# Performance work log

Hardware: AMD Instinct MI355X
Metric: run time of the kernel (lower is better)

Reference implementation:

```python
import jax, jax.numpy as jnp
import numpy as np

WIN = 20        # max-pooling window (win_size)
OFFSET = 40     # offset_d
TRUNC = 9       # trunc_window_size
SIGMA = 4.0     # gaussian sigma
SIL = 0         # sil_idx


def _smoothing_filter():
    h = TRUNC // 2
    x = jnp.arange(-h, h + 1, dtype=jnp.float32)
    g = jnp.exp(-0.5 * (x / SIGMA) ** 2)
    g = g / g.sum()
    f = jnp.zeros(WIN, jnp.float32)
    c = WIN // 2
    return f.at[c - h:c + h + 1].set(g)


def setup_inputs() -> dict:
    key = jax.random.key(0)
    k1, k2, k3, k4 = jax.random.split(key, 4)
    B, F, C, P = 32, 8192, 256, 256
    X = jax.nn.log_softmax(jax.random.normal(k1, (B, F, C), jnp.float32), axis=-1)
    lengths = jax.random.randint(k2, (B,), 4096, F + 1)
    p_end = lengths - 100                      # phoneme end well inside the utterance
    phoneme_nums = jax.random.randint(k3, (B,), 128, P + 1)
    tgt = jax.random.randint(k4, (B, P), 1, C)  # padded phoneme labels (avoid sil=0)
    return {"X": X, "lengths": lengths, "tgt": tgt, "p_end": p_end,
            "phoneme_nums": phoneme_nums}


def reference(X, lengths, tgt, p_end, phoneme_nums):
    B, F, C = X.shape
    P = tgt.shape[1]
    filt = _smoothing_filter()

    ends_ph = jnp.minimum(p_end + OFFSET, lengths)                      # [B]
    idxs = jnp.arange(P)[None, :]                                       # [1,P]
    starts = jnp.maximum(ends_ph[:, None] - WIN * (phoneme_nums[:, None] - idxs), 0)  # [B,P]
    ends = jnp.minimum(starts + WIN, lengths[:, None])                  # [B,P]

    t = jnp.arange(WIN)
    fidx = jnp.clip(starts[:, :, None] + t, 0, F - 1)
    b_idx = jnp.arange(B)[:, None, None]
    vals = X[b_idx, fidx, tgt[:, :, None]]

    wlen = ends - starts                                                # [B,P]
    valid_t = t[None, None, :] < wlen[:, :, None]
    vals = jnp.where(valid_t, vals, 0.0)  # zeros beyond window == torch zero-pad

    # torch F.conv1d(padding='same') with even kernel: pad left 9, right 10 (cross-corr)
    lpad = (WIN - 1) // 2
    padded = jnp.pad(vals, ((0, 0), (0, 0), (lpad, WIN - 1 - lpad)))
    smoothed = jax.lax.conv_general_dilated(
        padded.reshape(B * P, 1, -1), filt.reshape(1, 1, WIN),
        window_strides=(1,), padding='VALID').reshape(B, P, WIN)

    smoothed = jnp.where(valid_t, smoothed, -jnp.inf)
    ph_valid = idxs < phoneme_nums[:, None]                             # [B,P]
    loss = jnp.sum(jnp.where(ph_valid, -jnp.max(smoothed, axis=-1), 0.0))

    # silence penalty before first window and after last window
    first_start = starts[:, 0]                                          # [B]
    last_end = ends[jnp.arange(B), phoneme_nums - 1]                    # [B]
    tf = jnp.arange(F)[None, :]
    sil_mask = (tf < first_start[:, None]) | \
               ((tf >= last_end[:, None]) & (tf < lengths[:, None]))
    loss = loss - jnp.sum(jnp.where(sil_mask, X[:, :, SIL], 0.0))
    return loss
```

## Files before the change

### kernel.cpp

```cpp
#include <hip/hip_runtime.h>
#include <math.h>

#define WIN 20
#define OFFSET 40
#define B_ 32
#define F_ 8192
#define C_ 256
#define P_ 256
#define SIL_SPLIT 8

__global__ void zero_out_kernel(float* out) { out[0] = 0.0f; }

__global__ __launch_bounds__(256) void smoothed_loss_kernel(
    const float* __restrict__ X,
    const int* __restrict__ lengths,
    const int* __restrict__ tgt,
    const int* __restrict__ p_end,
    const int* __restrict__ phoneme_nums,
    float* __restrict__ out)
{
    __shared__ float sdata[4];
    const int tid = threadIdx.x;
    float contrib = 0.0f;

    if (blockIdx.x < B_) {
        const int b = blockIdx.x;
        const int pn = phoneme_nums[b];
        const int len = lengths[b];
        const int end_ph = min(p_end[b] + OFFSET, len);
        const int p = tid;
        if (p < pn) {
            const int start = max(end_ph - WIN * (pn - p), 0);
            const int end_  = min(start + WIN, len);
            const int wlen  = end_ - start;
            const int col   = tgt[b * P_ + p];
            const float* Xb = X + ((size_t)b * F_) * C_ + col;

            float vals[WIN];
            #pragma unroll
            for (int t = 0; t < WIN; ++t) {
                int f = start + t;
                f = min(max(f, 0), F_ - 1);
                vals[t] = (t < wlen) ? Xb[(size_t)f * C_] : 0.0f;
            }

            float g[9];
            float gs = 0.0f;
            #pragma unroll
            for (int i = 0; i < 9; ++i) {
                const float x = (float)(i - 4) * 0.25f;
                g[i] = __expf(-0.5f * x * x);
                gs += g[i];
            }
            const float inv = 1.0f / gs;

            float m = -INFINITY;
            for (int t = 0; t < wlen; ++t) {
                float s = 0.0f;
                #pragma unroll
                for (int i = 0; i < 9; ++i) {
                    const int j = t + i - 3;
                    const float v = (j >= 0 && j < WIN) ? vals[j] : 0.0f;
                    s = fmaf(g[i], v, s);
                }
                m = fmaxf(m, s * inv);
            }
            if (wlen > 0) contrib = -m;
        }
    } else {
        const int sb = blockIdx.x - B_;
        const int b  = sb / SIL_SPLIT;
        const int c  = sb % SIL_SPLIT;
        const int pn = phoneme_nums[b];
        const int len = lengths[b];
        const int end_ph = min(p_end[b] + OFFSET, len);
        const int first_start = max(end_ph - WIN * pn, 0);
        const int start_last  = max(end_ph - WIN, 0);
        const int last_end    = min(start_last + WIN, len);
        const float* Xb = X + (size_t)b * F_ * C_;

        float s = 0.0f;
        for (int f = c * 256 + tid; f < len; f += 256 * SIL_SPLIT) {
            const bool m = (f < first_start) | (f >= last_end);
            if (m) s += Xb[(size_t)f * C_];
        }
        contrib = -s;
    }

    #pragma unroll
    for (int off = 32; off > 0; off >>= 1)
        contrib += __shfl_down(contrib, off, 64);
    const int lane = tid & 63;
    const int wave = tid >> 6;
    if (lane == 0) sdata[wave] = contrib;
    __syncthreads();
    if (tid == 0) {
        const float tot = sdata[0] + sdata[1] + sdata[2] + sdata[3];
        atomicAdd(out, tot);
    }
}

extern "C" void kernel_launch(void* const* d_in, const int* in_sizes, int n_in,
                              void* d_out, int out_size, void* d_ws, size_t ws_size,
                              hipStream_t stream) {
    const float* X            = (const float*)d_in[0];
    const int* lengths        = (const int*)d_in[1];
    const int* tgt            = (const int*)d_in[2];
    const int* p_end          = (const int*)d_in[3];
    const int* phoneme_nums   = (const int*)d_in[4];
    float* out = (float*)d_out;

    zero_out_kernel<<<1, 1, 0, stream>>>(out);
    smoothed_loss_kernel<<<B_ + B_ * SIL_SPLIT, 256, 0, stream>>>(
        X, lengths, tgt, p_end, phoneme_nums, out);
}
```

Before: 320.0 us.

## Specialize full-window path, double silence split, replace zero kernel with memset

Adds a fast path for full-length windows that drops clamping and per-element bounds selects. The silence loop is unrolled into at most two loads per thread, with the number of silence blocks per batch doubled to 16. The zero-init kernel launch is replaced by hipMemsetAsync. The two-load silence code hard-codes F_ = 8192 and SIL_SPLIT = 16, and the runtime is likely dominated by strided gathers and launch overhead anyway.

```diff
diff --git a/kernel.cpp b/kernel.cpp
--- a/kernel.cpp
+++ b/kernel.cpp
@@ -7,9 +7,7 @@
 #define F_ 8192
 #define C_ 256
 #define P_ 256
-#define SIL_SPLIT 8
-
-__global__ void zero_out_kernel(float* out) { out[0] = 0.0f; }
+#define SIL_SPLIT 16
 
 __global__ __launch_bounds__(256) void smoothed_loss_kernel(
     const float* __restrict__ X,
@@ -34,14 +32,17 @@
             const int end_  = min(start + WIN, len);
             const int wlen  = end_ - start;
             const int col   = tgt[b * P_ + p];
-            const float* Xb = X + ((size_t)b * F_) * C_ + col;
+            const float* Xp = X + ((size_t)b * F_ + (size_t)start) * C_ + col;
 
             float vals[WIN];
-            #pragma unroll
-            for (int t = 0; t < WIN; ++t) {
-                int f = start + t;
-                f = min(max(f, 0), F_ - 1);
-                vals[t] = (t < wlen) ? Xb[(size_t)f * C_] : 0.0f;
+            if (wlen == WIN) {
+                #pragma unroll
+                for (int t = 0; t < WIN; ++t)
+                    vals[t] = Xp[(size_t)t * C_];
+            } else {
+                #pragma unroll
+                for (int t = 0; t < WIN; ++t)
+                    vals[t] = (t < wlen) ? Xp[(size_t)t * C_] : 0.0f;
             }
 
             float g[9];
@@ -55,22 +56,37 @@
             const float inv = 1.0f / gs;
 
             float m = -INFINITY;
-            for (int t = 0; t < wlen; ++t) {
-                float s = 0.0f;
+            if (wlen == WIN) {
                 #pragma unroll
-                for (int i = 0; i < 9; ++i) {
-                    const int j = t + i - 3;
-                    const float v = (j >= 0 && j < WIN) ? vals[j] : 0.0f;
-                    s = fmaf(g[i], v, s);
+                for (int t = 0; t < WIN; ++t) {
+                    float s = 0.0f;
+                    #pragma unroll
+                    for (int i = 0; i < 9; ++i) {
+                        const int j = t + i - 3;
+                        if (j >= 0 && j < WIN)
+                            s = fmaf(g[i], vals[j], s);
+                    }
+                    m = fmaxf(m, s * inv);
                 }
-                m = fmaxf(m, s * inv);
+                contrib = -m;
+            } else {
+                for (int t = 0; t < wlen; ++t) {
+                    float s = 0.0f;
+                    #pragma unroll
+                    for (int i = 0; i < 9; ++i) {
+                        const int j = t + i - 3;
+                        const float v = (j >= 0 && j < WIN) ? vals[j] : 0.0f;
+                        s = fmaf(g[i], v, s);
+                    }
+                    m = fmaxf(m, s * inv);
+                }
+                if (wlen > 0) contrib = -m;
             }
-            if (wlen > 0) contrib = -m;
         }
     } else {
         const int sb = blockIdx.x - B_;
-        const int b  = sb / SIL_SPLIT;
-        const int c  = sb % SIL_SPLIT;
+        const int b  = sb >> 4;
+        const int c  = sb & (SIL_SPLIT - 1);
         const int pn = phoneme_nums[b];
         const int len = lengths[b];
         const int end_ph = min(p_end[b] + OFFSET, len);
@@ -79,11 +95,13 @@
         const int last_end    = min(start_last + WIN, len);
         const float* Xb = X + (size_t)b * F_ * C_;
 
+        const int f0 = c * 256 + tid;
+        const int f1 = f0 + 256 * SIL_SPLIT;
         float s = 0.0f;
-        for (int f = c * 256 + tid; f < len; f += 256 * SIL_SPLIT) {
-            const bool m = (f < first_start) | (f >= last_end);
-            if (m) s += Xb[(size_t)f * C_];
-        }
+        if (f0 < len && ((f0 < first_start) | (f0 >= last_end)))
+            s += Xb[(size_t)f0 * C_];
+        if (f1 < len && ((f1 < first_start) | (f1 >= last_end)))
+            s += Xb[(size_t)f1 * C_];
         contrib = -s;
     }
 
@@ -110,7 +128,7 @@
     const int* phoneme_nums   = (const int*)d_in[4];
     float* out = (float*)d_out;
 
-    zero_out_kernel<<<1, 1, 0, stream>>>(out);
+    hipMemsetAsync(out, 0, sizeof(float), stream);
     smoothed_loss_kernel<<<B_ + B_ * SIL_SPLIT, 256, 0, stream>>>(
         X, lengths, tgt, p_end, phoneme_nums, out);
 }
```

After: 316.4 us. Within noise of the previous version (-1.1%).
